# Kernel tuning notes

Measured on AMD Instinct MI355X. Metric: run time of the kernel, lower is better.

## Reference

```python
import jax, jax.numpy as jnp
import numpy as np

N = 20000      # nodes
E = 320000     # edges (avg degree 16)
C = 64         # channels per degree
H = 8          # attention heads
DIM1 = 3       # degree-1 representation dim (2*1+1)
NUM_FEATURES = C * 1 + C * 3  # key_fiber.num_features = 256


def setup_inputs() -> dict:
    key = jax.random.key(0)
    ks = jax.random.split(key, 7)
    return {
        "value_0": jax.random.normal(ks[0], (E, C, 1), dtype=jnp.float32),
        "value_1": jax.random.normal(ks[1], (E, C, DIM1), dtype=jnp.float32),
        "key_0": jax.random.normal(ks[2], (E, C, 1), dtype=jnp.float32),
        "key_1": jax.random.normal(ks[3], (E, C, DIM1), dtype=jnp.float32),
        "query_0": jax.random.normal(ks[4], (N, C, 1), dtype=jnp.float32),
        "query_1": jax.random.normal(ks[5], (N, C, DIM1), dtype=jnp.float32),
        "dst": jax.random.randint(ks[6], (E,), 0, N),
    }


def _to_heads(f0, f1):
    # Fiber.to_attention_heads: per degree [n, C, dim] -> [n, H, (C//H)*dim], concat on last dim
    n = f0.shape[0]
    return jnp.concatenate([f0.reshape(n, H, -1), f1.reshape(n, H, -1)], axis=-1)


def reference(value_0, value_1, key_0, key_1, query_0, query_1, dst):
    k = _to_heads(key_0, key_1)        # [E, H, Dk]
    q = _to_heads(query_0, query_1)    # [N, H, Dk]
    # dgl.ops.e_dot_v: dot edge key with destination-node query, then scale
    logits = jnp.einsum('ehd,ehd->eh', k, q[dst]) / np.float32(np.sqrt(NUM_FEATURES))
    edge_prelogits = logits            # returned pre-softmax (scaled) as in original
    # edge_softmax over incoming edges of each destination node, per head
    m = jax.ops.segment_max(logits, dst, num_segments=N)           # [N, H]
    w = jnp.exp(logits - m[dst])                                   # [E, H]
    denom = jax.ops.segment_sum(w, dst, num_segments=N)            # [N, H]
    alpha = w / denom[dst]                                         # [E, H]

    def agg(v, dim):
        # value view: [E, H, C//H, dim]; weighted copy_e_sum -> [N, C, dim]
        vh = v.reshape(E, H, C // H, dim)
        out = jax.ops.segment_sum(alpha[:, :, None, None] * vh, dst, num_segments=N)
        return out.reshape(N, C, dim)

    out_0 = agg(value_0, 1)
    out_1 = agg(value_1, DIM1)
    return out_0, out_1, edge_prelogits
```

## Files before the change

### kernel.cpp

```cpp
#include <hip/hip_runtime.h>

#define N_NODES 20000
#define N_EDGES 320000
#define NEGF   -1e30f


__global__ __launch_bounds__(256) void k_zero(int* __restrict__ counts)
{
    int n = blockIdx.x * 256 + threadIdx.x;
    if (n < N_NODES) counts[n] = 0;
}

__global__ __launch_bounds__(256) void k_count(
    const int* __restrict__ dst, int* __restrict__ counts)
{
    int e = blockIdx.x * 256 + threadIdx.x;
    if (e < N_EDGES) atomicAdd(&counts[dst[e]], 1);
}

__global__ __launch_bounds__(1024) void k_scan(
    const int* __restrict__ counts, int* __restrict__ offsets,
    int* __restrict__ cursor)
{
    __shared__ int sm[1024];
    int t = threadIdx.x;
    int base = t * 20;
    int local[20];
    int s = 0;
    if (base < N_NODES) {
#pragma unroll
        for (int i = 0; i < 20; ++i) { local[i] = counts[base + i]; s += local[i]; }
    }
    sm[t] = s; __syncthreads();
    for (int off = 1; off < 1024; off <<= 1) {
        int x = (t >= off) ? sm[t - off] : 0;
        __syncthreads();
        sm[t] += x;
        __syncthreads();
    }
    int run = sm[t] - s;
    if (base < N_NODES) {
#pragma unroll
        for (int i = 0; i < 20; ++i) {
            offsets[base + i] = run; cursor[base + i] = run; run += local[i];
        }
    }
    if (t == 0) offsets[N_NODES] = N_EDGES;
}

__global__ __launch_bounds__(256) void k_fill(
    const int* __restrict__ dst, int* __restrict__ cursor, int* __restrict__ bucket)
{
    int e = blockIdx.x * 256 + threadIdx.x;
    if (e >= N_EDGES) return;
    int d = dst[e];
    int pos = atomicAdd(&cursor[d], 1);
    bucket[pos] = e;
}

#define DOT4(a,b) ((a).x*(b).x + (a).y*(b).y + (a).z*(b).z + (a).w*(b).w)
#define SC4(a,s)  { (a).x*=(s); (a).y*=(s); (a).z*=(s); (a).w*=(s); }
#define FMA4(a,s,p) { (a).x += (s)*(p).x; (a).y += (s)*(p).y; (a).z += (s)*(p).z; (a).w += (s)*(p).w; }
#define RED4(a,m) { (a).x += __shfl_xor((a).x,m); (a).y += __shfl_xor((a).y,m); \
                    (a).z += __shfl_xor((a).z,m); (a).w += __shfl_xor((a).w,m); }

__global__ __launch_bounds__(256) void k_fused(
    const float* __restrict__ v0, const float* __restrict__ v1,
    const float* __restrict__ k0, const float* __restrict__ k1,
    const float* __restrict__ q0, const float* __restrict__ q1,
    const int* __restrict__ offsets, const int* __restrict__ bucket,
    float* __restrict__ logits, float* __restrict__ out0, float* __restrict__ out1)
{
    int w = threadIdx.x >> 6;
    int l = threadIdx.x & 63;
    int node = blockIdx.x * 4 + w;

    int rs = offsets[node], re = offsets[node + 1];
    int deg = re - rs;

    int h = l & 7, slot8 = l >> 3, s2 = l >> 4, c = l & 15;
    int hv0  = c >> 1;
    int hv1a = c / 6;
    int hv1b = (c + 16) / 6;
    int hv1c = (c + 32) / 6;

    const float4* qh0 = (const float4*)(q0 + (size_t)node * 64  + h * 8);
    const float4* qh1 = (const float4*)(q1 + (size_t)node * 192 + h * 24);
    float4 Q0a = qh0[0], Q0b = qh0[1];
    float4 Q1a = qh1[0], Q1b = qh1[1], Q1c = qh1[2];
    float4 Q1d = qh1[3], Q1e = qh1[4], Q1f = qh1[5];

    int eL = 0;
    if (l < deg) eL = bucket[rs + l];

    float M = NEGF, S = 0.f;
    float4 a0  = {0,0,0,0}, a1a = {0,0,0,0}, a1b = {0,0,0,0}, a1c = {0,0,0,0};

    for (int base = 0; base < deg; base += 8) {
        int sA = base + slot8;
        bool okA = sA < deg;
        int iA = okA ? sA : 0;
        int eA = (iA < 64) ? __shfl(eL, iA) : bucket[rs + iA];

        int sB0 = base + s2, sB1 = base + s2 + 4;
        int iB0 = (sB0 < deg) ? sB0 : 0;
        int iB1 = (sB1 < deg) ? sB1 : 0;
        int eB0 = (iB0 < 64) ? __shfl(eL, iB0) : bucket[rs + iB0];
        int eB1 = (iB1 < 64) ? __shfl(eL, iB1) : bucket[rs + iB1];

        const float4* kr0 = (const float4*)(k0 + (size_t)eA * 64  + h * 8);
        const float4* kr1 = (const float4*)(k1 + (size_t)eA * 192 + h * 24);
        float4 K0a = kr0[0], K0b = kr0[1];
        float4 K1a = kr1[0], K1b = kr1[1], K1c = kr1[2];
        float4 K1d = kr1[3], K1e = kr1[4], K1f = kr1[5];

        const float4* v0A = (const float4*)(v0 + (size_t)eB0 * 64);
        const float4* v1A = (const float4*)(v1 + (size_t)eB0 * 192);
        const float4* v0B = (const float4*)(v0 + (size_t)eB1 * 64);
        const float4* v1B = (const float4*)(v1 + (size_t)eB1 * 192);
        float4 P0A = v0A[c], PaA = v1A[c], PbA = v1A[c + 16], PcA = v1A[c + 32];
        float4 P0B = v0B[c], PaB = v1B[c], PbB = v1B[c + 16], PcB = v1B[c + 32];

        float acc = DOT4(K0a, Q0a) + DOT4(K0b, Q0b)
                  + DOT4(K1a, Q1a) + DOT4(K1b, Q1b) + DOT4(K1c, Q1c)
                  + DOT4(K1d, Q1d) + DOT4(K1e, Q1e) + DOT4(K1f, Q1f);
        float x = okA ? acc * 0.0625f : NEGF;
        if (okA) logits[(size_t)eA * 8 + h] = x;

        float gM = x;
        gM = fmaxf(gM, __shfl_xor(gM, 8));
        gM = fmaxf(gM, __shfl_xor(gM, 16));
        gM = fmaxf(gM, __shfl_xor(gM, 32));
        float Mn = fmaxf(M, gM);
        float atil = okA ? __expf(x - Mn) : 0.f;
        float gS = atil;
        gS += __shfl_xor(gS, 8);
        gS += __shfl_xor(gS, 16);
        gS += __shfl_xor(gS, 32);
        float sc = __expf(M - Mn);
        S = S * sc + gS;
        M = Mn;

        float sc0 = __shfl(sc, hv0);
        float sca = __shfl(sc, hv1a);
        float scb = __shfl(sc, hv1b);
        float scc = __shfl(sc, hv1c);
        SC4(a0, sc0); SC4(a1a, sca); SC4(a1b, scb); SC4(a1c, scc);

        float l0A = __shfl(atil, s2 * 8 + hv0);
        float laA = __shfl(atil, s2 * 8 + hv1a);
        float lbA = __shfl(atil, s2 * 8 + hv1b);
        float lcA = __shfl(atil, s2 * 8 + hv1c);
        float l0B = __shfl(atil, (s2 + 4) * 8 + hv0);
        float laB = __shfl(atil, (s2 + 4) * 8 + hv1a);
        float lbB = __shfl(atil, (s2 + 4) * 8 + hv1b);
        float lcB = __shfl(atil, (s2 + 4) * 8 + hv1c);
        FMA4(a0, l0A, P0A); FMA4(a1a, laA, PaA); FMA4(a1b, lbA, PbA); FMA4(a1c, lcA, PcA);
        FMA4(a0, l0B, P0B); FMA4(a1a, laB, PaB); FMA4(a1b, lbB, PbB); FMA4(a1c, lcB, PcB);
    }

    float rinv = (S > 0.f) ? 1.f / S : 0.f;
    float r0 = __shfl(rinv, hv0);
    float ra = __shfl(rinv, hv1a);
    float rb = __shfl(rinv, hv1b);
    float rc = __shfl(rinv, hv1c);

    RED4(a0, 16); RED4(a0, 32);
    RED4(a1a, 16); RED4(a1a, 32);
    RED4(a1b, 16); RED4(a1b, 32);
    RED4(a1c, 16); RED4(a1c, 32);

    if (l < 16) {
        SC4(a0, r0); SC4(a1a, ra); SC4(a1b, rb); SC4(a1c, rc);
        float4* o0 = (float4*)(out0 + (size_t)node * 64);
        float4* o1 = (float4*)(out1 + (size_t)node * 192);
        o0[c]      = a0;
        o1[c]      = a1a;
        o1[c + 16] = a1b;
        o1[c + 32] = a1c;
    }
}

extern "C" void kernel_launch(void* const* d_in, const int* in_sizes, int n_in,
                              void* d_out, int out_size, void* d_ws, size_t ws_size,
                              hipStream_t stream) {
    const float* v0 = (const float*)d_in[0];
    const float* v1 = (const float*)d_in[1];
    const float* k0 = (const float*)d_in[2];
    const float* k1 = (const float*)d_in[3];
    const float* q0 = (const float*)d_in[4];
    const float* q1 = (const float*)d_in[5];
    const int*  dst = (const int*)d_in[6];

    float* out0   = (float*)d_out;
    float* out1   = out0 + (size_t)N_NODES * 64;
    float* logits = out1 + (size_t)N_NODES * 192;

    int* wsI     = (int*)d_ws;
    int* counts  = wsI;
    int* offsets = wsI + 20000;
    int* cursor  = wsI + 40064;
    int* bucket  = wsI + 60192;

    k_zero  <<<79,    256,  0, stream>>>(counts);
    k_count <<<1250,  256,  0, stream>>>(dst, counts);
    k_scan  <<<1,     1024, 0, stream>>>(counts, offsets, cursor);
    k_fill  <<<1250,  256,  0, stream>>>(dst, cursor, bucket);
    k_fused <<<5000,  256,  0, stream>>>(v0, v1, k0, k1, q0, q1,
                                         offsets, bucket, logits, out0, out1);
}
```

Measured before the change: 203.7 us.

## Stage key/value rows into LDS via async global_load_lds per chunk

Each wave now stages the key and value rows of a chunk of 8 edges into shared memory using global_load_lds, with 64 lanes each copying 16 bytes so that one row per tensor pair is contiguous. It waits on vmcnt and then reads K and V from LDS, replacing the direct per-lane global gathers. Launch bounds now request 2 blocks per CU to accommodate about 66KB of LDS per block. The aim is fully coalesced row loads issued up front, at the cost of an explicit full wait with no double-buffering, lower occupancy, and extra LDS traffic.

```diff
diff --git a/kernel.cpp b/kernel.cpp
--- a/kernel.cpp
+++ b/kernel.cpp
@@ -3,6 +3,8 @@
 #define N_NODES 20000
 #define N_EDGES 320000
 #define NEGF   -1e30f
+#define ROWF   260
+#define CHUNK  8
 
 
 __global__ __launch_bounds__(256) void k_zero(int* __restrict__ counts)
@@ -64,15 +66,31 @@
 #define RED4(a,m) { (a).x += __shfl_xor((a).x,m); (a).y += __shfl_xor((a).y,m); \
                     (a).z += __shfl_xor((a).z,m); (a).w += __shfl_xor((a).w,m); }
 
-__global__ __launch_bounds__(256) void k_fused(
+typedef __attribute__((address_space(3))) float       lds_f;
+typedef const __attribute__((address_space(1))) float gbl_f;
+
+__device__ __forceinline__ void stage_row(const float* g0, const float* g1,
+                                          float* dst, int lane)
+{
+    const float* src = (lane < 16) ? (g0 + lane * 4) : (g1 + (lane - 16) * 4);
+    __builtin_amdgcn_global_load_lds(
+        (const __attribute__((address_space(1))) void*)(gbl_f*)(uintptr_t)src,
+        (__attribute__((address_space(3))) void*)(lds_f*)(uintptr_t)dst,
+        16, 0, 0);
+}
+
+__global__ __launch_bounds__(256, 2) void k_fused(
     const float* __restrict__ v0, const float* __restrict__ v1,
     const float* __restrict__ k0, const float* __restrict__ k1,
     const float* __restrict__ q0, const float* __restrict__ q1,
     const int* __restrict__ offsets, const int* __restrict__ bucket,
     float* __restrict__ logits, float* __restrict__ out0, float* __restrict__ out1)
 {
+    __shared__ float smem[4 * 2 * CHUNK * ROWF];
     int w = threadIdx.x >> 6;
     int l = threadIdx.x & 63;
+    float* kbuf = smem + w * (2 * CHUNK * ROWF);
+    float* vbuf = kbuf + CHUNK * ROWF;
     int node = blockIdx.x * 4 + w;
 
     int rs = offsets[node], re = offsets[node + 1];
@@ -96,30 +114,34 @@
     float M = NEGF, S = 0.f;
     float4 a0  = {0,0,0,0}, a1a = {0,0,0,0}, a1b = {0,0,0,0}, a1c = {0,0,0,0};
 
-    for (int base = 0; base < deg; base += 8) {
-        int sA = base + slot8;
+    for (int cb = 0; cb < deg; cb += CHUNK) {
+        int rem = deg - cb;
+
+#pragma unroll
+        for (int s = 0; s < CHUNK; ++s) {
+            if (s < rem) {
+                int idx = cb + s;
+                int es = (idx < 64) ? __shfl(eL, idx) : bucket[rs + idx];
+                stage_row(k0 + (size_t)es * 64, k1 + (size_t)es * 192,
+                          kbuf + s * ROWF, l);
+                stage_row(v0 + (size_t)es * 64, v1 + (size_t)es * 192,
+                          vbuf + s * ROWF, l);
+            }
+        }
+        asm volatile("s_waitcnt vmcnt(0)" ::: "memory");
+        __builtin_amdgcn_sched_barrier(0);
+
+        int sA = cb + slot8;
         bool okA = sA < deg;
         int iA = okA ? sA : 0;
         int eA = (iA < 64) ? __shfl(eL, iA) : bucket[rs + iA];
 
-        int sB0 = base + s2, sB1 = base + s2 + 4;
-        int iB0 = (sB0 < deg) ? sB0 : 0;
-        int iB1 = (sB1 < deg) ? sB1 : 0;
-        int eB0 = (iB0 < 64) ? __shfl(eL, iB0) : bucket[rs + iB0];
-        int eB1 = (iB1 < 64) ? __shfl(eL, iB1) : bucket[rs + iB1];
-
-        const float4* kr0 = (const float4*)(k0 + (size_t)eA * 64  + h * 8);
-        const float4* kr1 = (const float4*)(k1 + (size_t)eA * 192 + h * 24);
-        float4 K0a = kr0[0], K0b = kr0[1];
-        float4 K1a = kr1[0], K1b = kr1[1], K1c = kr1[2];
-        float4 K1d = kr1[3], K1e = kr1[4], K1f = kr1[5];
-
-        const float4* v0A = (const float4*)(v0 + (size_t)eB0 * 64);
-        const float4* v1A = (const float4*)(v1 + (size_t)eB0 * 192);
-        const float4* v0B = (const float4*)(v0 + (size_t)eB1 * 64);
-        const float4* v1B = (const float4*)(v1 + (size_t)eB1 * 192);
-        float4 P0A = v0A[c], PaA = v1A[c], PbA = v1A[c + 16], PcA = v1A[c + 32];
-        float4 P0B = v0B[c], PaB = v1B[c], PbB = v1B[c + 16], PcB = v1B[c + 32];
+        const float* kr  = kbuf + slot8 * ROWF;
+        const float4* kv = (const float4*)kr;
+        float4 K0a = kv[h * 2], K0b = kv[h * 2 + 1];
+        const float4* kv1 = (const float4*)(kr + 64);
+        float4 K1a = kv1[h * 6 + 0], K1b = kv1[h * 6 + 1], K1c = kv1[h * 6 + 2];
+        float4 K1d = kv1[h * 6 + 3], K1e = kv1[h * 6 + 4], K1f = kv1[h * 6 + 5];
 
         float acc = DOT4(K0a, Q0a) + DOT4(K0b, Q0b)
                   + DOT4(K1a, Q1a) + DOT4(K1b, Q1b) + DOT4(K1c, Q1c)
@@ -155,8 +177,20 @@
         float laB = __shfl(atil, (s2 + 4) * 8 + hv1a);
         float lbB = __shfl(atil, (s2 + 4) * 8 + hv1b);
         float lcB = __shfl(atil, (s2 + 4) * 8 + hv1c);
-        FMA4(a0, l0A, P0A); FMA4(a1a, laA, PaA); FMA4(a1b, lbA, PbA); FMA4(a1c, lcA, PcA);
-        FMA4(a0, l0B, P0B); FMA4(a1a, laB, PaB); FMA4(a1b, lbB, PbB); FMA4(a1c, lcB, PcB);
+
+        const float4* vrA = (const float4*)(vbuf + s2 * ROWF);
+        const float4* vrB = (const float4*)(vbuf + (s2 + 4) * ROWF);
+        float4 P0A = vrA[c], PaA = vrA[16 + c], PbA = vrA[32 + c], PcA = vrA[48 + c];
+        float4 P0B = vrB[c], PaB = vrB[16 + c], PbB = vrB[32 + c], PcB = vrB[48 + c];
+
+        if (cb + s2 < deg) {
+            FMA4(a0, l0A, P0A); FMA4(a1a, laA, PaA);
+            FMA4(a1b, lbA, PbA); FMA4(a1c, lcA, PcA);
+        }
+        if (cb + s2 + 4 < deg) {
+            FMA4(a0, l0B, P0B); FMA4(a1a, laB, PaB);
+            FMA4(a1b, lbB, PbB); FMA4(a1c, lcB, PcB);
+        }
     }
 
     float rinv = (S > 0.f) ? 1.f / S : 0.f;
```

Measured after the change: 255.2 us. 1.25x slower.

## Split fused attention kernel into logits/softmax-stats pass and aggregation pass

Applied to the files above, without the earlier changes.

Replaces the single online-softmax kernel with two kernels. The first computes edge logits and per-node, per-head max and reciprocal sum, stored in workspace tables. The second re-reads the logits and recomputes the normalized weights while gathering value rows. This removes the serial rescale and shuffle chain from the aggregation loop and unrolls both loops for more memory-level parallelism. The cost is an extra launch plus writing and re-reading the logits and stats tables.

```diff
diff --git a/kernel.cpp b/kernel.cpp
--- a/kernel.cpp
+++ b/kernel.cpp
@@ -59,30 +59,43 @@
 }
 
 #define DOT4(a,b) ((a).x*(b).x + (a).y*(b).y + (a).z*(b).z + (a).w*(b).w)
-#define SC4(a,s)  { (a).x*=(s); (a).y*=(s); (a).z*=(s); (a).w*=(s); }
 #define FMA4(a,s,p) { (a).x += (s)*(p).x; (a).y += (s)*(p).y; (a).z += (s)*(p).z; (a).w += (s)*(p).w; }
 #define RED4(a,m) { (a).x += __shfl_xor((a).x,m); (a).y += __shfl_xor((a).y,m); \
                     (a).z += __shfl_xor((a).z,m); (a).w += __shfl_xor((a).w,m); }
-
-__global__ __launch_bounds__(256) void k_fused(
-    const float* __restrict__ v0, const float* __restrict__ v1,
+#define SC4(a,s)  { (a).x*=(s); (a).y*=(s); (a).z*=(s); (a).w*=(s); }
+
+
+#define A_BLOCK(BOFF, X0, X1)                                                   \
+{                                                                               \
+    int s0 = (BOFF) + slot8, s1 = s0 + 8;                                       \
+    int e0 = __shfl(eL, min(s0, deg - 1));                                      \
+    int e1 = __shfl(eL, min(s1, deg - 1));                                      \
+    const float4* ka0 = (const float4*)(k0 + (size_t)e0 * 64  + h * 8);         \
+    const float4* kb0 = (const float4*)(k1 + (size_t)e0 * 192 + h * 24);        \
+    const float4* ka1 = (const float4*)(k0 + (size_t)e1 * 64  + h * 8);         \
+    const float4* kb1 = (const float4*)(k1 + (size_t)e1 * 192 + h * 24);        \
+    float4 A0=ka0[0],A1=ka0[1],A2=kb0[0],A3=kb0[1],A4=kb0[2],A5=kb0[3],A6=kb0[4],A7=kb0[5]; \
+    float4 B0=ka1[0],B1=ka1[1],B2=kb1[0],B3=kb1[1],B4=kb1[2],B5=kb1[3],B6=kb1[4],B7=kb1[5]; \
+    float d0 = DOT4(A0,Q0a)+DOT4(A1,Q0b)+DOT4(A2,Q1a)+DOT4(A3,Q1b)              \
+             + DOT4(A4,Q1c)+DOT4(A5,Q1d)+DOT4(A6,Q1e)+DOT4(A7,Q1f);             \
+    float d1 = DOT4(B0,Q0a)+DOT4(B1,Q0b)+DOT4(B2,Q1a)+DOT4(B3,Q1b)              \
+             + DOT4(B4,Q1c)+DOT4(B5,Q1d)+DOT4(B6,Q1e)+DOT4(B7,Q1f);             \
+    if (s0 < deg) { X0 = d0 * 0.0625f; logits[(size_t)e0 * 8 + h] = X0; }       \
+    if (s1 < deg) { X1 = d1 * 0.0625f; logits[(size_t)e1 * 8 + h] = X1; }       \
+}
+
+__global__ __launch_bounds__(256) void k_logits_sm(
     const float* __restrict__ k0, const float* __restrict__ k1,
     const float* __restrict__ q0, const float* __restrict__ q1,
     const int* __restrict__ offsets, const int* __restrict__ bucket,
-    float* __restrict__ logits, float* __restrict__ out0, float* __restrict__ out1)
-{
-    int w = threadIdx.x >> 6;
-    int l = threadIdx.x & 63;
+    float* __restrict__ logits, float* __restrict__ Mtab, float* __restrict__ Rtab)
+{
+    int w = threadIdx.x >> 6, l = threadIdx.x & 63;
     int node = blockIdx.x * 4 + w;
-
     int rs = offsets[node], re = offsets[node + 1];
     int deg = re - rs;
-
-    int h = l & 7, slot8 = l >> 3, s2 = l >> 4, c = l & 15;
-    int hv0  = c >> 1;
-    int hv1a = c / 6;
-    int hv1b = (c + 16) / 6;
-    int hv1c = (c + 32) / 6;
+    if (deg == 0) return;
+    int h = l & 7, slot8 = l >> 3;
 
     const float4* qh0 = (const float4*)(q0 + (size_t)node * 64  + h * 8);
     const float4* qh1 = (const float4*)(q1 + (size_t)node * 192 + h * 24);
@@ -90,88 +103,136 @@
     float4 Q1a = qh1[0], Q1b = qh1[1], Q1c = qh1[2];
     float4 Q1d = qh1[3], Q1e = qh1[4], Q1f = qh1[5];
 
-    int eL = 0;
-    if (l < deg) eL = bucket[rs + l];
-
-    float M = NEGF, S = 0.f;
-    float4 a0  = {0,0,0,0}, a1a = {0,0,0,0}, a1b = {0,0,0,0}, a1c = {0,0,0,0};
-
-    for (int base = 0; base < deg; base += 8) {
-        int sA = base + slot8;
-        bool okA = sA < deg;
-        int iA = okA ? sA : 0;
-        int eA = (iA < 64) ? __shfl(eL, iA) : bucket[rs + iA];
-
-        int sB0 = base + s2, sB1 = base + s2 + 4;
-        int iB0 = (sB0 < deg) ? sB0 : 0;
-        int iB1 = (sB1 < deg) ? sB1 : 0;
-        int eB0 = (iB0 < 64) ? __shfl(eL, iB0) : bucket[rs + iB0];
-        int eB1 = (iB1 < 64) ? __shfl(eL, iB1) : bucket[rs + iB1];
-
-        const float4* kr0 = (const float4*)(k0 + (size_t)eA * 64  + h * 8);
-        const float4* kr1 = (const float4*)(k1 + (size_t)eA * 192 + h * 24);
-        float4 K0a = kr0[0], K0b = kr0[1];
-        float4 K1a = kr1[0], K1b = kr1[1], K1c = kr1[2];
-        float4 K1d = kr1[3], K1e = kr1[4], K1f = kr1[5];
-
-        const float4* v0A = (const float4*)(v0 + (size_t)eB0 * 64);
-        const float4* v1A = (const float4*)(v1 + (size_t)eB0 * 192);
-        const float4* v0B = (const float4*)(v0 + (size_t)eB1 * 64);
-        const float4* v1B = (const float4*)(v1 + (size_t)eB1 * 192);
-        float4 P0A = v0A[c], PaA = v1A[c], PbA = v1A[c + 16], PcA = v1A[c + 32];
-        float4 P0B = v0B[c], PaB = v1B[c], PbB = v1B[c + 16], PcB = v1B[c + 32];
-
-        float acc = DOT4(K0a, Q0a) + DOT4(K0b, Q0b)
-                  + DOT4(K1a, Q1a) + DOT4(K1b, Q1b) + DOT4(K1c, Q1c)
-                  + DOT4(K1d, Q1d) + DOT4(K1e, Q1e) + DOT4(K1f, Q1f);
-        float x = okA ? acc * 0.0625f : NEGF;
-        if (okA) logits[(size_t)eA * 8 + h] = x;
-
-        float gM = x;
-        gM = fmaxf(gM, __shfl_xor(gM, 8));
-        gM = fmaxf(gM, __shfl_xor(gM, 16));
-        gM = fmaxf(gM, __shfl_xor(gM, 32));
-        float Mn = fmaxf(M, gM);
-        float atil = okA ? __expf(x - Mn) : 0.f;
-        float gS = atil;
-        gS += __shfl_xor(gS, 8);
-        gS += __shfl_xor(gS, 16);
-        gS += __shfl_xor(gS, 32);
-        float sc = __expf(M - Mn);
-        S = S * sc + gS;
-        M = Mn;
-
-        float sc0 = __shfl(sc, hv0);
-        float sca = __shfl(sc, hv1a);
-        float scb = __shfl(sc, hv1b);
-        float scc = __shfl(sc, hv1c);
-        SC4(a0, sc0); SC4(a1a, sca); SC4(a1b, scb); SC4(a1c, scc);
-
-        float l0A = __shfl(atil, s2 * 8 + hv0);
-        float laA = __shfl(atil, s2 * 8 + hv1a);
-        float lbA = __shfl(atil, s2 * 8 + hv1b);
-        float lcA = __shfl(atil, s2 * 8 + hv1c);
-        float l0B = __shfl(atil, (s2 + 4) * 8 + hv0);
-        float laB = __shfl(atil, (s2 + 4) * 8 + hv1a);
-        float lbB = __shfl(atil, (s2 + 4) * 8 + hv1b);
-        float lcB = __shfl(atil, (s2 + 4) * 8 + hv1c);
-        FMA4(a0, l0A, P0A); FMA4(a1a, laA, PaA); FMA4(a1b, lbA, PbA); FMA4(a1c, lcA, PcA);
-        FMA4(a0, l0B, P0B); FMA4(a1a, laB, PaB); FMA4(a1b, lbB, PbB); FMA4(a1c, lcB, PcB);
-    }
-
-    float rinv = (S > 0.f) ? 1.f / S : 0.f;
-    float r0 = __shfl(rinv, hv0);
-    float ra = __shfl(rinv, hv1a);
-    float rb = __shfl(rinv, hv1b);
-    float rc = __shfl(rinv, hv1c);
-
-    RED4(a0, 16); RED4(a0, 32);
+    if (deg <= 64) {
+        int eL = bucket[rs + min(l, deg - 1)];
+        float x0=NEGF,x1=NEGF,x2=NEGF,x3=NEGF,x4=NEGF,x5=NEGF,x6=NEGF,x7=NEGF;
+        A_BLOCK(0, x0, x1)
+        if (deg > 16) A_BLOCK(16, x2, x3)
+        if (deg > 32) A_BLOCK(32, x4, x5)
+        if (deg > 48) A_BLOCK(48, x6, x7)
+
+        float M = fmaxf(fmaxf(fmaxf(x0,x1),fmaxf(x2,x3)),
+                        fmaxf(fmaxf(x4,x5),fmaxf(x6,x7)));
+        M = fmaxf(M, __shfl_xor(M, 8));
+        M = fmaxf(M, __shfl_xor(M, 16));
+        M = fmaxf(M, __shfl_xor(M, 32));
+        float S = __expf(x0-M)+__expf(x1-M)+__expf(x2-M)+__expf(x3-M)
+                + __expf(x4-M)+__expf(x5-M)+__expf(x6-M)+__expf(x7-M);
+        S += __shfl_xor(S, 8);
+        S += __shfl_xor(S, 16);
+        S += __shfl_xor(S, 32);
+        if (slot8 == 0) {
+            Mtab[node * 8 + h] = M;
+            Rtab[node * 8 + h] = 1.f / S;
+        }
+    } else {
+        float M = NEGF, S = 0.f;
+        for (int cb = 0; cb < deg; cb += 8) {
+            int s = cb + slot8;
+            bool ok = s < deg;
+            int e = bucket[rs + min(s, deg - 1)];
+            const float4* ka = (const float4*)(k0 + (size_t)e * 64  + h * 8);
+            const float4* kb = (const float4*)(k1 + (size_t)e * 192 + h * 24);
+            float4 A0=ka[0],A1=ka[1],A2=kb[0],A3=kb[1],A4=kb[2],A5=kb[3],A6=kb[4],A7=kb[5];
+            float d = DOT4(A0,Q0a)+DOT4(A1,Q0b)+DOT4(A2,Q1a)+DOT4(A3,Q1b)
+                    + DOT4(A4,Q1c)+DOT4(A5,Q1d)+DOT4(A6,Q1e)+DOT4(A7,Q1f);
+            float x = ok ? d * 0.0625f : NEGF;
+            if (ok) logits[(size_t)e * 8 + h] = x;
+            float gM = x;
+            gM = fmaxf(gM, __shfl_xor(gM, 8));
+            gM = fmaxf(gM, __shfl_xor(gM, 16));
+            gM = fmaxf(gM, __shfl_xor(gM, 32));
+            float Mn = fmaxf(M, gM);
+            float p = ok ? __expf(x - Mn) : 0.f;
+            float gS = p;
+            gS += __shfl_xor(gS, 8);
+            gS += __shfl_xor(gS, 16);
+            gS += __shfl_xor(gS, 32);
+            S = S * __expf(M - Mn) + gS;
+            M = Mn;
+        }
+        if (slot8 == 0) {
+            Mtab[node * 8 + h] = M;
+            Rtab[node * 8 + h] = 1.f / S;
+        }
+    }
+}
+
+
+#define B_BODY(BASE)                                                            \
+{                                                                               \
+    int sA = (BASE) + s2, sB = (BASE) + s2 + 4;                                 \
+    int pA = rs + min(sA, deg - 1), pB = rs + min(sB, deg - 1);                 \
+    int eA = bucket[pA], eB = bucket[pB];                                       \
+    const float* lrA = logits + (size_t)eA * 8;                                 \
+    const float* lrB = logits + (size_t)eB * 8;                                 \
+    float xA0 = lrA[hv0], xAa = lrA[hv1a], xAb = lrA[hv1b], xAc = lrA[hv1c];    \
+    float xB0 = lrB[hv0], xBa = lrB[hv1a], xBb = lrB[hv1b], xBc = lrB[hv1c];    \
+    const float4* r0A = (const float4*)(v0 + (size_t)eA * 64);                  \
+    const float4* r1A = (const float4*)(v1 + (size_t)eA * 192);                 \
+    const float4* r0B = (const float4*)(v0 + (size_t)eB * 64);                  \
+    const float4* r1B = (const float4*)(v1 + (size_t)eB * 192);                 \
+    float4 P0A = r0A[c], PaA = r1A[c], PbA = r1A[c + 16], PcA = r1A[c + 32];    \
+    float4 P0B = r0B[c], PaB = r1B[c], PbB = r1B[c + 16], PcB = r1B[c + 32];    \
+    float wA0 = __expf(xA0 - M0) * R0, wAa = __expf(xAa - Ma) * Ra;             \
+    float wAb = __expf(xAb - Mb) * Rb, wAc = __expf(xAc - Mc) * Rc;             \
+    float wB0 = __expf(xB0 - M0) * R0, wBa = __expf(xBa - Ma) * Ra;             \
+    float wBb = __expf(xBb - Mb) * Rb, wBc = __expf(xBc - Mc) * Rc;             \
+    if (sA >= deg) { wA0 = wAa = wAb = wAc = 0.f; }                             \
+    if (sB >= deg) { wB0 = wBa = wBb = wBc = 0.f; }                             \
+    FMA4(a0, wA0, P0A); FMA4(a1a, wAa, PaA); FMA4(a1b, wAb, PbA); FMA4(a1c, wAc, PcA); \
+    FMA4(a0, wB0, P0B); FMA4(a1a, wBa, PaB); FMA4(a1b, wBb, PbB); FMA4(a1c, wBc, PcB); \
+}
+
+__global__ __launch_bounds__(256) void k_agg(
+    const float* __restrict__ v0, const float* __restrict__ v1,
+    const float* __restrict__ logits, const int* __restrict__ offsets,
+    const int* __restrict__ bucket,
+    const float* __restrict__ Mtab, const float* __restrict__ Rtab,
+    float* __restrict__ out0, float* __restrict__ out1)
+{
+    int w = threadIdx.x >> 6, l = threadIdx.x & 63;
+    int node = blockIdx.x * 4 + w;
+    int rs = offsets[node], deg = offsets[node + 1] - rs;
+    int s2 = l >> 4, c = l & 15;
+
+    if (deg == 0) {
+        if (l < 16) {
+            float4 z = {0,0,0,0};
+            ((float4*)(out0 + (size_t)node * 64))[c] = z;
+            float4* o1 = (float4*)(out1 + (size_t)node * 192);
+            o1[c] = z; o1[c + 16] = z; o1[c + 32] = z;
+        }
+        return;
+    }
+
+    int hv0  = c >> 1;
+    int hv1a = c / 6;
+    int hv1b = (c + 16) / 6;
+    int hv1c = (c + 32) / 6;
+    float M0 = Mtab[node * 8 + hv0],  R0 = Rtab[node * 8 + hv0];
+    float Ma = Mtab[node * 8 + hv1a], Ra = Rtab[node * 8 + hv1a];
+    float Mb = Mtab[node * 8 + hv1b], Rb = Rtab[node * 8 + hv1b];
+    float Mc = Mtab[node * 8 + hv1c], Rc = Rtab[node * 8 + hv1c];
+
+    float4 a0 = {0,0,0,0}, a1a = {0,0,0,0}, a1b = {0,0,0,0}, a1c = {0,0,0,0};
+
+    B_BODY(0)
+    if (deg > 8)  B_BODY(8)
+    if (deg > 16) B_BODY(16)
+    if (deg > 24) B_BODY(24)
+    if (deg > 32) B_BODY(32)
+    if (deg > 40) B_BODY(40)
+    if (deg > 48) B_BODY(48)
+    if (deg > 56) B_BODY(56)
+    for (int base = 64; base < deg; base += 8) B_BODY(base)
+
+    RED4(a0, 16);  RED4(a0, 32);
     RED4(a1a, 16); RED4(a1a, 32);
     RED4(a1b, 16); RED4(a1b, 32);
     RED4(a1c, 16); RED4(a1c, 32);
 
     if (l < 16) {
-        SC4(a0, r0); SC4(a1a, ra); SC4(a1b, rb); SC4(a1c, rc);
         float4* o0 = (float4*)(out0 + (size_t)node * 64);
         float4* o1 = (float4*)(out1 + (size_t)node * 192);
         o0[c]      = a0;
@@ -196,16 +257,20 @@
     float* out1   = out0 + (size_t)N_NODES * 64;
     float* logits = out1 + (size_t)N_NODES * 192;
 
-    int* wsI     = (int*)d_ws;
-    int* counts  = wsI;
-    int* offsets = wsI + 20000;
-    int* cursor  = wsI + 40064;
-    int* bucket  = wsI + 60192;
-
-    k_zero  <<<79,    256,  0, stream>>>(counts);
-    k_count <<<1250,  256,  0, stream>>>(dst, counts);
-    k_scan  <<<1,     1024, 0, stream>>>(counts, offsets, cursor);
-    k_fill  <<<1250,  256,  0, stream>>>(dst, cursor, bucket);
-    k_fused <<<5000,  256,  0, stream>>>(v0, v1, k0, k1, q0, q1,
-                                         offsets, bucket, logits, out0, out1);
-}
+    int* wsI       = (int*)d_ws;
+    int* counts    = wsI;
+    int* offsets   = wsI + 20000;
+    int* cursor    = wsI + 40064;
+    int* bucket    = wsI + 60192;
+    float* Mtab    = (float*)(wsI + 380192);
+    float* Rtab    = (float*)(wsI + 540192);
+
+    k_zero      <<<79,   256,  0, stream>>>(counts);
+    k_count     <<<1250, 256,  0, stream>>>(dst, counts);
+    k_scan      <<<1,    1024, 0, stream>>>(counts, offsets, cursor);
+    k_fill      <<<1250, 256,  0, stream>>>(dst, cursor, bucket);
+    k_logits_sm <<<5000, 256,  0, stream>>>(k0, k1, q0, q1, offsets, bucket,
+                                            logits, Mtab, Rtab);
+    k_agg       <<<5000, 256,  0, stream>>>(v0, v1, logits, offsets, bucket,
+                                            Mtab, Rtab, out0, out1);
+}
```

After: 202.9 us. Within noise of the previous version (-0.4%).
